# Kernel tuning notes

Hardware: AMD Instinct MI355X
Metric: run time of the kernel (lower is better)

## Reference

```python
import jax, jax.numpy as jnp
import numpy as np

IN_FEATURES = 4096
OUT_FEATURES = 4096
IN_GROUP = 8
OUT_GROUP = 1
NUM_CODEBOOKS = 1
CODEBOOK_SIZE = 2 ** 16
NUM_OUT_GROUPS = OUT_FEATURES // OUT_GROUP   # 4096
NUM_IN_GROUPS = IN_FEATURES // IN_GROUP      # 512


def setup_inputs() -> dict:
    key = jax.random.key(0)
    k1, k2, k3, k4, k5 = jax.random.split(key, 5)
    input = jax.random.normal(k1, (4, 2048, IN_FEATURES), dtype=jnp.float32)
    codes = jax.random.randint(k2, (NUM_OUT_GROUPS, NUM_IN_GROUPS, NUM_CODEBOOKS), 0, CODEBOOK_SIZE, dtype=jnp.int32)
    codebooks = jax.random.normal(k3, (NUM_CODEBOOKS, CODEBOOK_SIZE, OUT_GROUP, IN_GROUP), dtype=jnp.float32)
    scales = jax.random.uniform(k4, (NUM_OUT_GROUPS, 1, 1, 1), dtype=jnp.float32)
    bias = jax.random.normal(k5, (OUT_FEATURES,), dtype=jnp.float32)
    return {"input": input, "codes": codes, "codebooks": codebooks, "scales": scales, "bias": bias}


def _dequantize_weight(codes, codebooks, scales):
    # codes: [nog, nig, nc] int; codebooks: [nc, K, og, ig]; scales: [nog, 1, 1, 1]
    nc = codebooks.shape[0]
    # gather per-codebook entries: [nog, nig, nc, og, ig]
    gathered = codebooks[jnp.arange(nc), codes]
    # sum over codebooks, apply per-out-group scale -> [nog, nig, og, ig]
    w = gathered.sum(axis=2) * scales
    nog, nig, og, ig = w.shape
    # [nog, og, nig, ig] -> [out_features, in_features]
    return w.transpose(0, 2, 1, 3).reshape(nog * og, nig * ig)


def reference(input, codes, codebooks, scales, bias):
    # Faithful AQLM dequant-GEMM: reconstruct W then input @ W^T + bias
    W = _dequantize_weight(codes, codebooks, scales)  # [out, in]
    out = jnp.einsum("bso,io->bsi", input, W.T.T) if False else input @ W.T
    if bias is not None:
        out = out + bias
    return out
```

## Files before the change

kernel.cpp:

```cpp
#include <hip/hip_runtime.h>
#include <hip/hip_bf16.h>
#include <stdint.h>

#define M_DIM 8192
#define N_DIM 4096
#define K_DIM 4096
#define NOG   4096
#define NIG   512

typedef __bf16 bf16;
typedef __attribute__((ext_vector_type(8))) __bf16 bf16x8;
typedef __attribute__((ext_vector_type(4))) float f32x4;


__device__ __forceinline__ void gload16(const void* g, void* lds) {
    __builtin_amdgcn_global_load_lds(
        (__attribute__((address_space(1))) void*)g,
        (__attribute__((address_space(3))) void*)lds,
        16 , 0 , 0 );
}

__global__ __launch_bounds__(256) void k_convert_tile(const float* __restrict__ in,
                                                      bf16* __restrict__ out) {
    __shared__ __align__(16) bf16 tile[256 * 8];
    const int t   = threadIdx.x;
    const int g   = blockIdx.y;
    const int h0  = blockIdx.x * 4;
    const int row = t >> 4;
    const int cc  = t & 15;
    const float4* p = (const float4*)(in + (size_t)(g * 16 + row) * K_DIM
                                         + h0 * 32 + cc * 8);
    float4 a = p[0], b = p[1];
    bf16x8 v;
    v[0] = (bf16)a.x; v[1] = (bf16)a.y; v[2] = (bf16)a.z; v[3] = (bf16)a.w;
    v[4] = (bf16)b.x; v[5] = (bf16)b.y; v[6] = (bf16)b.z; v[7] = (bf16)b.w;
    const int widx = (cc >> 2) * 64 + (cc & 3) * 16 + row;
    ((bf16x8*)tile)[widx] = v;
    __syncthreads();
    bf16x8 o = ((bf16x8*)tile)[t];
    ((bf16x8*)out)[((size_t)g * 128 + h0) * 64 + t] = o;
}

__global__ __launch_bounds__(256) void k_dequant_tile(const int* __restrict__ codes,
                                                      const float* __restrict__ cb,
                                                      const float* __restrict__ scales,
                                                      bf16* __restrict__ w) {
    const int t    = threadIdx.x;
    const int gB   = blockIdx.y;
    const int h0   = blockIdx.x * 4;
    const int hl   = t >> 6;
    const int kblk = (t >> 4) & 3;
    const int row  = t & 15;
    const int o    = gB * 16 + row;
    const int iG   = blockIdx.x * 16 + hl * 4 + kblk;
    unsigned code = (unsigned)codes[o * NIG + iG];
    float s = scales[o];
    const float4* e = (const float4*)(cb + (size_t)code * 8);
    float4 e0 = e[0], e1 = e[1];
    bf16x8 v;
    v[0] = (bf16)(e0.x * s); v[1] = (bf16)(e0.y * s);
    v[2] = (bf16)(e0.z * s); v[3] = (bf16)(e0.w * s);
    v[4] = (bf16)(e1.x * s); v[5] = (bf16)(e1.y * s);
    v[6] = (bf16)(e1.z * s); v[7] = (bf16)(e1.w * s);
    ((bf16x8*)w)[((size_t)gB * 128 + h0) * 64 + t] = v;
}

#define BM 256
#define BN 256
#define BK 64
#define KSTEPS (K_DIM / BK)

__device__ __forceinline__ void gemm_phase(
    const bf16* __restrict__ AsR, const bf16* __restrict__ BsR,
    bf16* __restrict__ AsW, bf16* __restrict__ BsW,
    const bf16* paw0, const bf16* paw1, const bf16* pbw0, const bf16* pbw1,
    int gA0, int gB0, int lane, const int h, int ss,
    f32x4 (&acc)[8][4])
{
    bf16x8 af[8], bq[4];
    #pragma unroll
    for (int m = 0; m < 8; ++m)
        af[m] = *(const bf16x8*)(AsR + (size_t)(gA0 + m) * 1024 + h * 512 + lane * 8);
    #pragma unroll
    for (int j = 0; j < 4; ++j)
        bq[j] = *(const bf16x8*)(BsR + (size_t)(gB0 + j) * 1024 + h * 512 + lane * 8);

    if (ss < 128) {
        gload16(paw0 + (size_t)ss * 512, AsW + h * 512);
        gload16(paw1 + (size_t)ss * 512, AsW + 1024 + h * 512);
        gload16(pbw0 + (size_t)ss * 512, BsW + h * 512);
        gload16(pbw1 + (size_t)ss * 512, BsW + 1024 + h * 512);
    }

    asm volatile("s_waitcnt vmcnt(4)" ::: "memory");
    __builtin_amdgcn_s_barrier();
    asm volatile("s_waitcnt lgkmcnt(0)" ::: "memory");
    __builtin_amdgcn_sched_barrier(0);

    __builtin_amdgcn_s_setprio(1);
    #pragma unroll
    for (int i = 0; i < 8; ++i)
        #pragma unroll
        for (int j = 0; j < 4; ++j)
            acc[i][j] = __builtin_amdgcn_mfma_f32_16x16x32_bf16(
                af[i], bq[j], acc[i][j], 0, 0, 0);
    __builtin_amdgcn_s_setprio(0);
    __builtin_amdgcn_s_barrier();
}

__global__ __launch_bounds__(512, 2) void k_gemm_tiled(
    const bf16* __restrict__ A,
    const bf16* __restrict__ B,
    const float* __restrict__ bias,
    float* __restrict__ C)
{
    __shared__ __align__(16) bf16 As[2][16 * 1024];
    __shared__ __align__(16) bf16 Bs[2][16 * 1024];

    const int tid  = threadIdx.x;
    const int wave = tid >> 6;
    const int lane = tid & 63;
    const int quad = lane >> 4;
    const int l16  = lane & 15;

    const int bn0 = blockIdx.x * BN;
    const int bm0 = blockIdx.y * BM;
    const int wm  = (wave >> 2) * 128;
    const int wn  = (wave & 3) * 64;
    const int gA0 = (wave >> 2) * 8;
    const int gB0 = (wave & 3) * 4;

    const bf16* paw0 = A + ((size_t)(blockIdx.y * 16 + wave * 2 + 0) * 8192 + lane) * 8;
    const bf16* paw1 = A + ((size_t)(blockIdx.y * 16 + wave * 2 + 1) * 8192 + lane) * 8;
    const bf16* pbw0 = B + ((size_t)(blockIdx.x * 16 + wave * 2 + 0) * 8192 + lane) * 8;
    const bf16* pbw1 = B + ((size_t)(blockIdx.x * 16 + wave * 2 + 1) * 8192 + lane) * 8;

    bf16* As0w = &As[0][wave * 2048];
    bf16* As1w = &As[1][wave * 2048];
    bf16* Bs0w = &Bs[0][wave * 2048];
    bf16* Bs1w = &Bs[1][wave * 2048];

    gload16(paw0,       As0w);        gload16(paw1,       As0w + 1024);
    gload16(pbw0,       Bs0w);        gload16(pbw1,       Bs0w + 1024);
    gload16(paw0 + 512, As0w + 512);  gload16(paw1 + 512, As0w + 1536);
    gload16(pbw0 + 512, Bs0w + 512);  gload16(pbw1 + 512, Bs0w + 1536);
    asm volatile("s_waitcnt vmcnt(4)" ::: "memory");
    __builtin_amdgcn_s_barrier();

    f32x4 acc[8][4] = {};

    const bf16* AsR0 = &As[0][0]; const bf16* BsR0 = &Bs[0][0];
    const bf16* AsR1 = &As[1][0]; const bf16* BsR1 = &Bs[1][0];

    for (int ks = 0; ks < KSTEPS; ks += 2) {
        const int s0 = ks * 2;
        gemm_phase(AsR0, BsR0, As1w, Bs1w, paw0, paw1, pbw0, pbw1,
                   gA0, gB0, lane, 0, s0 + 2, acc);
        gemm_phase(AsR0, BsR0, As1w, Bs1w, paw0, paw1, pbw0, pbw1,
                   gA0, gB0, lane, 1, s0 + 3, acc);
        gemm_phase(AsR1, BsR1, As0w, Bs0w, paw0, paw1, pbw0, pbw1,
                   gA0, gB0, lane, 0, s0 + 4, acc);
        gemm_phase(AsR1, BsR1, As0w, Bs0w, paw0, paw1, pbw0, pbw1,
                   gA0, gB0, lane, 1, s0 + 5, acc);
    }

    #pragma unroll
    for (int j = 0; j < 4; ++j) {
        const int gn = bn0 + wn + j * 16 + l16;
        const float bz = bias[gn];
        #pragma unroll
        for (int i = 0; i < 8; ++i) {
            float* cp = C + (size_t)(bm0 + wm + i * 16 + quad * 4) * N_DIM + gn;
            #pragma unroll
            for (int r = 0; r < 4; ++r)
                cp[(size_t)r * N_DIM] = acc[i][j][r] + bz;
        }
    }
}

extern "C" void kernel_launch(void* const* d_in, const int* in_sizes, int n_in,
                              void* d_out, int out_size, void* d_ws, size_t ws_size,
                              hipStream_t stream) {
    const float* input     = (const float*)d_in[0];
    const int*   codes     = (const int*)d_in[1];
    const float* codebooks = (const float*)d_in[2];
    const float* scales    = (const float*)d_in[3];
    const float* bias      = (const float*)d_in[4];
    float* out = (float*)d_out;

    bf16* Abf = (bf16*)d_ws;
    bf16* Wbf = (bf16*)((char*)d_ws + (size_t)M_DIM * K_DIM * sizeof(bf16));

    (void)in_sizes; (void)n_in; (void)out_size; (void)ws_size;

    {
        dim3 g(K_DIM / 128, M_DIM / 16);
        k_convert_tile<<<g, 256, 0, stream>>>(input, Abf);
    }
    {
        dim3 g(K_DIM / 128, NOG / 16);
        k_dequant_tile<<<g, 256, 0, stream>>>(codes, codebooks, scales, Wbf);
    }
    {
        dim3 g(N_DIM / BN, M_DIM / BM);
        k_gemm_tiled<<<g, 512, 0, stream>>>(Abf, Wbf, bias, out);
    }
}
```

Baseline: 457.5 us.

## Replace double-buffered GEMM loop with 4-slot LDS ring and register double-buffering

Restructures the GEMM main loop from two LDS buffers into a four-slot ring of K=32 slices, staged three slices ahead. Fragment reads for the next slice are issued before the MFMA cluster of the current slice, using two alternating register sets, so LDS reads overlap matrix math. The per-phase barrier count drops from two to one. It also remaps block indices with a swizzle so concurrently running blocks share A/B tiles in cache. The cost is more registers for the second fragment set and delicate waitcnt accounting, which could break correctness or hurt occupancy.

```diff
diff --git a/kernel.cpp b/kernel.cpp
--- a/kernel.cpp
+++ b/kernel.cpp
@@ -67,36 +67,34 @@
 
 #define BM 256
 #define BN 256
-#define BK 64
-#define KSTEPS (K_DIM / BK)
-
-__device__ __forceinline__ void gemm_phase(
-    const bf16* __restrict__ AsR, const bf16* __restrict__ BsR,
-    bf16* __restrict__ AsW, bf16* __restrict__ BsW,
-    const bf16* paw0, const bf16* paw1, const bf16* pbw0, const bf16* pbw1,
-    int gA0, int gB0, int lane, const int h, int ss,
-    f32x4 (&acc)[8][4])
-{
-    bf16x8 af[8], bq[4];
+#define NSLICE (K_DIM / 32)
+
+__device__ __forceinline__ void ds_read_frags(
+    const bf16* slot, int gA0, int gB0, int lane,
+    bf16x8 (&af)[8], bf16x8 (&bq)[4])
+{
     #pragma unroll
     for (int m = 0; m < 8; ++m)
-        af[m] = *(const bf16x8*)(AsR + (size_t)(gA0 + m) * 1024 + h * 512 + lane * 8);
+        af[m] = *(const bf16x8*)(slot + (gA0 + m) * 512 + lane * 8);
     #pragma unroll
     for (int j = 0; j < 4; ++j)
-        bq[j] = *(const bf16x8*)(BsR + (size_t)(gB0 + j) * 1024 + h * 512 + lane * 8);
-
-    if (ss < 128) {
-        gload16(paw0 + (size_t)ss * 512, AsW + h * 512);
-        gload16(paw1 + (size_t)ss * 512, AsW + 1024 + h * 512);
-        gload16(pbw0 + (size_t)ss * 512, BsW + h * 512);
-        gload16(pbw1 + (size_t)ss * 512, BsW + 1024 + h * 512);
-    }
-
-    asm volatile("s_waitcnt vmcnt(4)" ::: "memory");
-    __builtin_amdgcn_s_barrier();
-    asm volatile("s_waitcnt lgkmcnt(0)" ::: "memory");
-    __builtin_amdgcn_sched_barrier(0);
-
+        bq[j] = *(const bf16x8*)(slot + 8192 + (gB0 + j) * 512 + lane * 8);
+}
+
+__device__ __forceinline__ void stage_slice(
+    bf16* slot, const bf16* pa0, const bf16* pa1,
+    const bf16* pb0, const bf16* pb1, int w2, int ss)
+{
+    const size_t off = (size_t)ss * 512;
+    gload16(pa0 + off, slot + (w2 + 0) * 512);
+    gload16(pa1 + off, slot + (w2 + 1) * 512);
+    gload16(pb0 + off, slot + 8192 + (w2 + 0) * 512);
+    gload16(pb1 + off, slot + 8192 + (w2 + 1) * 512);
+}
+
+__device__ __forceinline__ void mfma_cluster(
+    const bf16x8 (&af)[8], const bf16x8 (&bq)[4], f32x4 (&acc)[8][4])
+{
     __builtin_amdgcn_s_setprio(1);
     #pragma unroll
     for (int i = 0; i < 8; ++i)
@@ -105,7 +103,6 @@
             acc[i][j] = __builtin_amdgcn_mfma_f32_16x16x32_bf16(
                 af[i], bq[j], acc[i][j], 0, 0, 0);
     __builtin_amdgcn_s_setprio(0);
-    __builtin_amdgcn_s_barrier();
 }
 
 __global__ __launch_bounds__(512, 2) void k_gemm_tiled(
@@ -114,55 +111,85 @@
     const float* __restrict__ bias,
     float* __restrict__ C)
 {
-    __shared__ __align__(16) bf16 As[2][16 * 1024];
-    __shared__ __align__(16) bf16 Bs[2][16 * 1024];
+    __shared__ __align__(16) bf16 ring[4][16384];
 
     const int tid  = threadIdx.x;
     const int wave = tid >> 6;
     const int lane = tid & 63;
     const int quad = lane >> 4;
     const int l16  = lane & 15;
-
-    const int bn0 = blockIdx.x * BN;
-    const int bm0 = blockIdx.y * BM;
+    const int w2   = wave * 2;
+
+    const int bhw = blockIdx.y * 16 + blockIdx.x;
+    const int bsz = (bhw & 7) * 64 + (bhw >> 3);
+    const int bx  = bsz & 15;
+    const int by  = bsz >> 4;
+
+    const int bn0 = bx * BN;
+    const int bm0 = by * BM;
     const int wm  = (wave >> 2) * 128;
     const int wn  = (wave & 3) * 64;
     const int gA0 = (wave >> 2) * 8;
     const int gB0 = (wave & 3) * 4;
 
-    const bf16* paw0 = A + ((size_t)(blockIdx.y * 16 + wave * 2 + 0) * 8192 + lane) * 8;
-    const bf16* paw1 = A + ((size_t)(blockIdx.y * 16 + wave * 2 + 1) * 8192 + lane) * 8;
-    const bf16* pbw0 = B + ((size_t)(blockIdx.x * 16 + wave * 2 + 0) * 8192 + lane) * 8;
-    const bf16* pbw1 = B + ((size_t)(blockIdx.x * 16 + wave * 2 + 1) * 8192 + lane) * 8;
-
-    bf16* As0w = &As[0][wave * 2048];
-    bf16* As1w = &As[1][wave * 2048];
-    bf16* Bs0w = &Bs[0][wave * 2048];
-    bf16* Bs1w = &Bs[1][wave * 2048];
-
-    gload16(paw0,       As0w);        gload16(paw1,       As0w + 1024);
-    gload16(pbw0,       Bs0w);        gload16(pbw1,       Bs0w + 1024);
-    gload16(paw0 + 512, As0w + 512);  gload16(paw1 + 512, As0w + 1536);
-    gload16(pbw0 + 512, Bs0w + 512);  gload16(pbw1 + 512, Bs0w + 1536);
+    const bf16* pa0 = A + ((size_t)(by * 16 + w2 + 0) * 8192 + lane) * 8;
+    const bf16* pa1 = A + ((size_t)(by * 16 + w2 + 1) * 8192 + lane) * 8;
+    const bf16* pb0 = B + ((size_t)(bx * 16 + w2 + 0) * 8192 + lane) * 8;
+    const bf16* pb1 = B + ((size_t)(bx * 16 + w2 + 1) * 8192 + lane) * 8;
+
+    f32x4 acc[8][4] = {};
+    bf16x8 afA[8], bqA[4], afB[8], bqB[4];
+
+    stage_slice(&ring[0][0], pa0, pa1, pb0, pb1, w2, 0);
+    stage_slice(&ring[1][0], pa0, pa1, pb0, pb1, w2, 1);
+    stage_slice(&ring[2][0], pa0, pa1, pb0, pb1, w2, 2);
     asm volatile("s_waitcnt vmcnt(4)" ::: "memory");
     __builtin_amdgcn_s_barrier();
-
-    f32x4 acc[8][4] = {};
-
-    const bf16* AsR0 = &As[0][0]; const bf16* BsR0 = &Bs[0][0];
-    const bf16* AsR1 = &As[1][0]; const bf16* BsR1 = &Bs[1][0];
-
-    for (int ks = 0; ks < KSTEPS; ks += 2) {
-        const int s0 = ks * 2;
-        gemm_phase(AsR0, BsR0, As1w, Bs1w, paw0, paw1, pbw0, pbw1,
-                   gA0, gB0, lane, 0, s0 + 2, acc);
-        gemm_phase(AsR0, BsR0, As1w, Bs1w, paw0, paw1, pbw0, pbw1,
-                   gA0, gB0, lane, 1, s0 + 3, acc);
-        gemm_phase(AsR1, BsR1, As0w, Bs0w, paw0, paw1, pbw0, pbw1,
-                   gA0, gB0, lane, 0, s0 + 4, acc);
-        gemm_phase(AsR1, BsR1, As0w, Bs0w, paw0, paw1, pbw0, pbw1,
-                   gA0, gB0, lane, 1, s0 + 5, acc);
-    }
+    __builtin_amdgcn_sched_barrier(0);
+    ds_read_frags(&ring[0][0], gA0, gB0, lane, afA, bqA);
+    __builtin_amdgcn_sched_barrier(0);
+
+#define PHASE(RD, ST, SS, AFC, BQC, AFN, BQN)                                \
+    ds_read_frags(&ring[RD][0], gA0, gB0, lane, AFN, BQN);                   \
+    stage_slice(&ring[ST][0], pa0, pa1, pb0, pb1, w2, (SS));                 \
+    asm volatile("s_waitcnt lgkmcnt(12)" ::: "memory");                      \
+    __builtin_amdgcn_sched_barrier(0);                                       \
+    mfma_cluster(AFC, BQC, acc);                                             \
+    asm volatile("s_waitcnt vmcnt(4)" ::: "memory");                         \
+    __builtin_amdgcn_s_barrier();                                            \
+    __builtin_amdgcn_sched_barrier(0);
+
+    for (int t = 0; t < 31; ++t) {
+        const int s0 = t * 4;
+        PHASE(1, 3, s0 + 3, afA, bqA, afB, bqB);
+        PHASE(2, 0, s0 + 4, afB, bqB, afA, bqA);
+        PHASE(3, 1, s0 + 5, afA, bqA, afB, bqB);
+        PHASE(0, 2, s0 + 6, afB, bqB, afA, bqA);
+    }
+
+    ds_read_frags(&ring[1][0], gA0, gB0, lane, afB, bqB);
+    stage_slice(&ring[3][0], pa0, pa1, pb0, pb1, w2, 127);
+    asm volatile("s_waitcnt lgkmcnt(12)" ::: "memory");
+    __builtin_amdgcn_sched_barrier(0);
+    mfma_cluster(afA, bqA, acc);
+    asm volatile("s_waitcnt vmcnt(4)" ::: "memory");
+    __builtin_amdgcn_s_barrier();
+    __builtin_amdgcn_sched_barrier(0);
+    ds_read_frags(&ring[2][0], gA0, gB0, lane, afA, bqA);
+    asm volatile("s_waitcnt lgkmcnt(12)" ::: "memory");
+    __builtin_amdgcn_sched_barrier(0);
+    mfma_cluster(afB, bqB, acc);
+    asm volatile("s_waitcnt vmcnt(0)" ::: "memory");
+    __builtin_amdgcn_s_barrier();
+    __builtin_amdgcn_sched_barrier(0);
+    ds_read_frags(&ring[3][0], gA0, gB0, lane, afB, bqB);
+    asm volatile("s_waitcnt lgkmcnt(12)" ::: "memory");
+    __builtin_amdgcn_sched_barrier(0);
+    mfma_cluster(afA, bqA, acc);
+    asm volatile("s_waitcnt lgkmcnt(0)" ::: "memory");
+    __builtin_amdgcn_sched_barrier(0);
+    mfma_cluster(afB, bqB, acc);
+#undef PHASE
 
     #pragma unroll
     for (int j = 0; j < 4; ++j) {
```

After: 495.6 us. 8.3% more time.

## Restructure GEMM main loop into quadrant-split 8-phase pipeline with block swizzle

Applied to the files above, without the earlier changes.

Rewrites the GEMM K-loop to split each 64-wide K tile into A/B halves. Each wave reads and multiplies 4x2 sub-quadrants in eight phases per two K tiles, interleaving global-to-LDS staging with MFMA bursts so register fragments are reused across phases. It also remaps block indices to group blocks for better L2 reuse, and swizzles LDS chunk indices in the convert kernel to avoid bank conflicts. This adds more barriers per K tile and a complex staging order that must stay hazard-free, which costs synchronisation overhead.

```diff
diff --git a/kernel.cpp b/kernel.cpp
--- a/kernel.cpp
+++ b/kernel.cpp
@@ -18,6 +18,10 @@
         (__attribute__((address_space(1))) void*)g,
         (__attribute__((address_space(3))) void*)lds,
         16 , 0 , 0 );
+}
+
+__device__ __forceinline__ int chunk_swz(int i) {
+    return i ^ (((i >> 3) ^ (i >> 6)) & 7);
 }
 
 __global__ __launch_bounds__(256) void k_convert_tile(const float* __restrict__ in,
@@ -35,9 +39,9 @@
     v[0] = (bf16)a.x; v[1] = (bf16)a.y; v[2] = (bf16)a.z; v[3] = (bf16)a.w;
     v[4] = (bf16)b.x; v[5] = (bf16)b.y; v[6] = (bf16)b.z; v[7] = (bf16)b.w;
     const int widx = (cc >> 2) * 64 + (cc & 3) * 16 + row;
-    ((bf16x8*)tile)[widx] = v;
+    ((bf16x8*)tile)[chunk_swz(widx)] = v;
     __syncthreads();
-    bf16x8 o = ((bf16x8*)tile)[t];
+    bf16x8 o = ((bf16x8*)tile)[chunk_swz(t)];
     ((bf16x8*)out)[((size_t)g * 128 + h0) * 64 + t] = o;
 }
 
@@ -67,46 +71,7 @@
 
 #define BM 256
 #define BN 256
-#define BK 64
-#define KSTEPS (K_DIM / BK)
-
-__device__ __forceinline__ void gemm_phase(
-    const bf16* __restrict__ AsR, const bf16* __restrict__ BsR,
-    bf16* __restrict__ AsW, bf16* __restrict__ BsW,
-    const bf16* paw0, const bf16* paw1, const bf16* pbw0, const bf16* pbw1,
-    int gA0, int gB0, int lane, const int h, int ss,
-    f32x4 (&acc)[8][4])
-{
-    bf16x8 af[8], bq[4];
-    #pragma unroll
-    for (int m = 0; m < 8; ++m)
-        af[m] = *(const bf16x8*)(AsR + (size_t)(gA0 + m) * 1024 + h * 512 + lane * 8);
-    #pragma unroll
-    for (int j = 0; j < 4; ++j)
-        bq[j] = *(const bf16x8*)(BsR + (size_t)(gB0 + j) * 1024 + h * 512 + lane * 8);
-
-    if (ss < 128) {
-        gload16(paw0 + (size_t)ss * 512, AsW + h * 512);
-        gload16(paw1 + (size_t)ss * 512, AsW + 1024 + h * 512);
-        gload16(pbw0 + (size_t)ss * 512, BsW + h * 512);
-        gload16(pbw1 + (size_t)ss * 512, BsW + 1024 + h * 512);
-    }
-
-    asm volatile("s_waitcnt vmcnt(4)" ::: "memory");
-    __builtin_amdgcn_s_barrier();
-    asm volatile("s_waitcnt lgkmcnt(0)" ::: "memory");
-    __builtin_amdgcn_sched_barrier(0);
-
-    __builtin_amdgcn_s_setprio(1);
-    #pragma unroll
-    for (int i = 0; i < 8; ++i)
-        #pragma unroll
-        for (int j = 0; j < 4; ++j)
-            acc[i][j] = __builtin_amdgcn_mfma_f32_16x16x32_bf16(
-                af[i], bq[j], acc[i][j], 0, 0, 0);
-    __builtin_amdgcn_s_setprio(0);
-    __builtin_amdgcn_s_barrier();
-}
+#define KTILES (K_DIM / 64)
 
 __global__ __launch_bounds__(512, 2) void k_gemm_tiled(
     const bf16* __restrict__ A,
@@ -114,8 +79,8 @@
     const float* __restrict__ bias,
     float* __restrict__ C)
 {
-    __shared__ __align__(16) bf16 As[2][16 * 1024];
-    __shared__ __align__(16) bf16 Bs[2][16 * 1024];
+    __shared__ __align__(16) bf16 AL[2][2][8192];
+    __shared__ __align__(16) bf16 BL[2][2][8192];
 
     const int tid  = threadIdx.x;
     const int wave = tid >> 6;
@@ -123,46 +88,100 @@
     const int quad = lane >> 4;
     const int l16  = lane & 15;
 
-    const int bn0 = blockIdx.x * BN;
-    const int bm0 = blockIdx.y * BM;
+    const int bhw = blockIdx.y * 16 + blockIdx.x;
+    const int bsz = (bhw & 7) * 64 + (bhw >> 3);
+    const int bx  = bsz & 15;
+    const int by  = bsz >> 4;
+
+    const int bn0 = bx * BN;
+    const int bm0 = by * BM;
     const int wm  = (wave >> 2) * 128;
     const int wn  = (wave & 3) * 64;
-    const int gA0 = (wave >> 2) * 8;
-    const int gB0 = (wave & 3) * 4;
-
-    const bf16* paw0 = A + ((size_t)(blockIdx.y * 16 + wave * 2 + 0) * 8192 + lane) * 8;
-    const bf16* paw1 = A + ((size_t)(blockIdx.y * 16 + wave * 2 + 1) * 8192 + lane) * 8;
-    const bf16* pbw0 = B + ((size_t)(blockIdx.x * 16 + wave * 2 + 0) * 8192 + lane) * 8;
-    const bf16* pbw1 = B + ((size_t)(blockIdx.x * 16 + wave * 2 + 1) * 8192 + lane) * 8;
-
-    bf16* As0w = &As[0][wave * 2048];
-    bf16* As1w = &As[1][wave * 2048];
-    bf16* Bs0w = &Bs[0][wave * 2048];
-    bf16* Bs1w = &Bs[1][wave * 2048];
-
-    gload16(paw0,       As0w);        gload16(paw1,       As0w + 1024);
-    gload16(pbw0,       Bs0w);        gload16(pbw1,       Bs0w + 1024);
-    gload16(paw0 + 512, As0w + 512);  gload16(paw1 + 512, As0w + 1536);
-    gload16(pbw0 + 512, Bs0w + 512);  gload16(pbw1 + 512, Bs0w + 1536);
-    asm volatile("s_waitcnt vmcnt(4)" ::: "memory");
+
+    const int halfA = wave >> 2;
+    const int halfB = (wave & 3) >> 1;
+    const int bslot = (wave & 1) * 4;
+
+    const bf16* gA0 = A + ((size_t)(by * 16 + wave)      * 8192 + lane) * 8;
+    const bf16* gA1 = A + ((size_t)(by * 16 + 8 + wave)  * 8192 + lane) * 8;
+    const bf16* gB0 = B + ((size_t)(bx * 16 + wave)      * 8192 + lane) * 8;
+    const bf16* gB1 = B + ((size_t)(bx * 16 + 8 + wave)  * 8192 + lane) * 8;
+
+    f32x4 acc[8][4] = {};
+    bf16x8 afA[8], afB[8], bqA[4], bqB[4];
+
+#define STAGE_A(buf, half, kt) do { if ((kt) < KTILES) {                      \
+        const bf16* s_ = ((half) ? gA1 : gA0) + (size_t)(kt) * 1024;          \
+        bf16* d_ = &AL[buf][half][wave * 1024];                               \
+        gload16(s_, d_); gload16(s_ + 512, d_ + 512); } } while (0)
+#define STAGE_B(buf, half, kt) do { if ((kt) < KTILES) {                      \
+        const bf16* s_ = ((half) ? gB1 : gB0) + (size_t)(kt) * 1024;          \
+        bf16* d_ = &BL[buf][half][wave * 1024];                               \
+        gload16(s_, d_); gload16(s_ + 512, d_ + 512); } } while (0)
+#define READ_A(af, buf, mh) {                                                 \
+    _Pragma("unroll") for (int i_ = 0; i_ < 4; ++i_)                          \
+    _Pragma("unroll") for (int kk_ = 0; kk_ < 2; ++kk_)                       \
+        af[i_ * 2 + kk_] = *(const bf16x8*)(&AL[buf][halfA]                   \
+            [((mh) * 4 + i_) * 1024 + kk_ * 512 + lane * 8]); }
+#define READ_B(bq, buf, nh) {                                                 \
+    _Pragma("unroll") for (int j_ = 0; j_ < 2; ++j_)                          \
+    _Pragma("unroll") for (int kk_ = 0; kk_ < 2; ++kk_)                       \
+        bq[j_ * 2 + kk_] = *(const bf16x8*)(&BL[buf][halfB]                   \
+            [(bslot + (nh) * 2 + j_) * 1024 + kk_ * 512 + lane * 8]); }
+#define FENCE() do {                                                          \
+        asm volatile("s_waitcnt vmcnt(4)" ::: "memory");                      \
+        __builtin_amdgcn_s_barrier(); } while (0)
+#define MFMA16(af, bq, mh, nh) do {                                           \
+        asm volatile("s_waitcnt lgkmcnt(0)" ::: "memory");                    \
+        __builtin_amdgcn_sched_barrier(0);                                    \
+        __builtin_amdgcn_s_setprio(1);                                        \
+        _Pragma("unroll") for (int kk_ = 0; kk_ < 2; ++kk_)                   \
+        _Pragma("unroll") for (int i_ = 0; i_ < 4; ++i_)                      \
+        _Pragma("unroll") for (int j_ = 0; j_ < 2; ++j_)                      \
+            acc[(mh) * 4 + i_][(nh) * 2 + j_] =                               \
+                __builtin_amdgcn_mfma_f32_16x16x32_bf16(                      \
+                    af[i_ * 2 + kk_], bq[j_ * 2 + kk_],                       \
+                    acc[(mh) * 4 + i_][(nh) * 2 + j_], 0, 0, 0);              \
+        __builtin_amdgcn_s_setprio(0);                                        \
+        __builtin_amdgcn_s_barrier(); } while (0)
+
+    STAGE_B(0, 0, 0); STAGE_B(0, 1, 0);
+    STAGE_A(0, 0, 0); STAGE_A(0, 1, 0);
+    STAGE_B(1, 0, 1); STAGE_B(1, 1, 1);
+    asm volatile("s_waitcnt vmcnt(0)" ::: "memory");
     __builtin_amdgcn_s_barrier();
 
-    f32x4 acc[8][4] = {};
-
-    const bf16* AsR0 = &As[0][0]; const bf16* BsR0 = &Bs[0][0];
-    const bf16* AsR1 = &As[1][0]; const bf16* BsR1 = &Bs[1][0];
-
-    for (int ks = 0; ks < KSTEPS; ks += 2) {
-        const int s0 = ks * 2;
-        gemm_phase(AsR0, BsR0, As1w, Bs1w, paw0, paw1, pbw0, pbw1,
-                   gA0, gB0, lane, 0, s0 + 2, acc);
-        gemm_phase(AsR0, BsR0, As1w, Bs1w, paw0, paw1, pbw0, pbw1,
-                   gA0, gB0, lane, 1, s0 + 3, acc);
-        gemm_phase(AsR1, BsR1, As0w, Bs0w, paw0, paw1, pbw0, pbw1,
-                   gA0, gB0, lane, 0, s0 + 4, acc);
-        gemm_phase(AsR1, BsR1, As0w, Bs0w, paw0, paw1, pbw0, pbw1,
-                   gA0, gB0, lane, 1, s0 + 5, acc);
-    }
+    for (int t = 0; t < KTILES / 2; ++t) {
+        const int k1 = 2 * t + 1, k2 = 2 * t + 2, k3 = 2 * t + 3;
+        READ_A(afA, 0, 0); READ_B(bqA, 0, 0);
+        STAGE_A(1, 0, k1);
+        FENCE(); MFMA16(afA, bqA, 0, 0);
+        READ_B(bqB, 0, 1);
+        STAGE_A(1, 1, k1);
+        FENCE(); MFMA16(afA, bqB, 0, 1);
+        READ_A(afB, 0, 1);
+        STAGE_B(0, 0, k2);
+        FENCE(); MFMA16(afB, bqB, 1, 1);
+        STAGE_B(0, 1, k2);
+        FENCE(); MFMA16(afB, bqA, 1, 0);
+        READ_A(afA, 1, 0); READ_B(bqA, 1, 0);
+        STAGE_A(0, 0, k2);
+        FENCE(); MFMA16(afA, bqA, 0, 0);
+        READ_B(bqB, 1, 1);
+        STAGE_A(0, 1, k2);
+        FENCE(); MFMA16(afA, bqB, 0, 1);
+        READ_A(afB, 1, 1);
+        STAGE_B(1, 0, k3);
+        FENCE(); MFMA16(afB, bqB, 1, 1);
+        STAGE_B(1, 1, k3);
+        FENCE(); MFMA16(afB, bqA, 1, 0);
+    }
+#undef STAGE_A
+#undef STAGE_B
+#undef READ_A
+#undef READ_B
+#undef FENCE
+#undef MFMA16
 
     #pragma unroll
     for (int j = 0; j < 4; ++j) {
```

Result: no change. 460.4 us (+0.7%).
